# Performance work log

Measured on AMD Instinct MI355X. Metric: run time of the kernel, lower is better.

Reference implementation:

```python
import jax, jax.numpy as jnp
import numpy as np

N_NODES = 100000
N_EDGES = 1600000
D_IN = 128
D_HID = 256
D_OUT = 128


def _glorot(key, shape):
    fan_in, fan_out = shape[1], shape[0]
    lim = (6.0 / (fan_in + fan_out)) ** 0.5
    return jax.random.uniform(key, shape, jnp.float32, -lim, lim)


def setup_inputs() -> dict:
    key = jax.random.key(0)
    ks = jax.random.split(key, 8)
    x = jax.random.normal(ks[0], (N_NODES, D_IN), jnp.float32)
    edge_index = jax.random.randint(ks[1], (2, N_EDGES), 0, N_NODES, jnp.int32)
    return {
        "x": x,
        "edge_index": edge_index,
        # layer 1: in=D_IN -> D_HID
        "Wl1": _glorot(ks[2], (D_HID, D_IN)), "bl1": jnp.zeros((D_HID,), jnp.float32),
        "Wr1": _glorot(ks[3], (D_HID, D_IN)),
        # layer 2: D_HID -> D_HID
        "Wl2": _glorot(ks[4], (D_HID, D_HID)), "bl2": jnp.zeros((D_HID,), jnp.float32),
        "Wr2": _glorot(ks[5], (D_HID, D_HID)),
        # layer 3: D_HID -> D_OUT
        "Wl3": _glorot(ks[6], (D_OUT, D_HID)), "bl3": jnp.zeros((D_OUT,), jnp.float32),
        "Wr3": _glorot(ks[7], (D_OUT, D_HID)),
    }


def _sage_conv(x, src, dst, inv_deg, Wl, bl, Wr):
    # PyG SAGEConv (aggr='mean'): out = lin_l(mean_j x_j) + lin_r(x_i)
    agg = jax.ops.segment_sum(x[src], dst, num_segments=N_NODES)  # [N, F]
    mean = agg * inv_deg[:, None]
    return mean @ Wl.T + bl + x @ Wr.T


def reference(x, edge_index, Wl1, bl1, Wr1, Wl2, bl2, Wr2, Wl3, bl3, Wr3):
    src, dst = edge_index[0], edge_index[1]
    deg = jax.ops.segment_sum(jnp.ones((src.shape[0],), jnp.float32), dst,
                              num_segments=N_NODES)
    inv_deg = jnp.where(deg > 0, 1.0 / jnp.maximum(deg, 1.0), 0.0)
    h = jax.nn.relu(_sage_conv(x, src, dst, inv_deg, Wl1, bl1, Wr1))
    h = jax.nn.relu(_sage_conv(h, src, dst, inv_deg, Wl2, bl2, Wr2))
    return _sage_conv(h, src, dst, inv_deg, Wl3, bl3, Wr3)
```

## Files before the change

kernel.cpp:

```cpp
#include <hip/hip_runtime.h>

#define NN 100000
#define NE 1600000
#define DIN 128
#define DHID 256
#define DOUT 128
#define CAP 64

typedef unsigned int u32;
typedef unsigned short u16;

typedef __bf16 bf16x8 __attribute__((ext_vector_type(8)));
typedef float  f32x4  __attribute__((ext_vector_type(4)));

__device__ inline u16 f2bf(float f) {
    u32 u = __float_as_uint(f);
    u32 r = u + 0x7FFFu + ((u >> 16) & 1u);
    return (u16)(r >> 16);
}
__device__ inline u32 pack2(float a, float b) {
    return (u32)f2bf(a) | ((u32)f2bf(b) << 16);
}
__device__ inline float bflo(u32 u) { return __uint_as_float(u << 16); }
__device__ inline float bfhi(u32 u) { return __uint_as_float(u & 0xffff0000u); }

__global__ void csr_build(const int* __restrict__ src, const int* __restrict__ dst,
                          int* __restrict__ fill, int* __restrict__ csrC, int nE) {
    int g  = blockIdx.x & 7;
    int bg = blockIdx.x >> 3;
    int nbg = gridDim.x >> 3;
    int lo = g * (NN / 8), hi = lo + (NN / 8);
    for (int e = bg * 256 + threadIdx.x; e < nE; e += nbg * 256) {
        int d = __builtin_nontemporal_load(dst + e);
        if (d >= lo && d < hi) {
            int pos = atomicAdd(&fill[d], 1);
            if (pos < CAP) csrC[(size_t)d * CAP + pos] = __builtin_nontemporal_load(src + e);
        }
    }
}

__global__ void invdeg_from_fill(const int* __restrict__ fill, float* __restrict__ invdeg, int n) {
    int i = blockIdx.x * 256 + threadIdx.x;
    if (i < n) { int d = fill[i]; invdeg[i] = d > 0 ? 1.0f / (float)d : 0.0f; }
}

__global__ void f32_to_bf16(const float4* __restrict__ in, uint2* __restrict__ outp, int total4) {
    int i = blockIdx.x * 256 + threadIdx.x;
    if (i < total4) {
        float4 v = in[i];
        uint2 r; r.x = pack2(v.x, v.y); r.y = pack2(v.z, v.w);
        outp[i] = r;
    }
}

__global__ void weights_to_bf16(const float4* __restrict__ W0, const float4* __restrict__ W1,
                                const float4* __restrict__ W2, const float4* __restrict__ W3,
                                const float4* __restrict__ W4, const float4* __restrict__ W5,
                                uint2* __restrict__ outp) {
    int i = blockIdx.x * 256 + threadIdx.x;
    if (i >= 65536) return;
    const float4* p; int off;
    if (i < 8192)       { p = W0; off = i; }
    else if (i < 16384) { p = W1; off = i - 8192; }
    else if (i < 32768) { p = W2; off = i - 16384; }
    else if (i < 49152) { p = W3; off = i - 32768; }
    else if (i < 57344) { p = W4; off = i - 49152; }
    else                { p = W5; off = i - 57344; }
    float4 v = p[off];
    uint2 r; r.x = pack2(v.x, v.y); r.y = pack2(v.z, v.w);
    outp[i] = r;
}

#define ACC8(A, U) \
    A[0] += bflo(U.x); A[1] += bfhi(U.x); A[2] += bflo(U.y); A[3] += bfhi(U.y); \
    A[4] += bflo(U.z); A[5] += bfhi(U.z); A[6] += bflo(U.w); A[7] += bfhi(U.w);

__global__ __launch_bounds__(256)
void agg128_u4(const uint4* __restrict__ feat,
               const int* __restrict__ fill, const float* __restrict__ invdeg,
               const int* __restrict__ csrC, uint4* __restrict__ aggOut) {
    int w = (blockIdx.x * 256 + threadIdx.x) >> 6;
    int lane = threadIdx.x & 63;
    if (w >= NN) return;
    int dg = fill[w]; if (dg > CAP) dg = CAP;
    const int* cp = csrC + (size_t)w * CAP;
    int q = lane >> 4, sub = lane & 15;
    float a[8] = {0,0,0,0,0,0,0,0};
    float b[8] = {0,0,0,0,0,0,0,0};
    int j = 0;
    for (; j + 7 < dg; j += 8) {
        int s0 = cp[j + q], s1 = cp[j + 4 + q];
        uint4 u0 = feat[(size_t)s0 * 16 + sub];
        uint4 u1 = feat[(size_t)s1 * 16 + sub];
        ACC8(a, u0); ACC8(b, u1);
    }
    while (j < dg) {
        if (j + q < dg) {
            int s0 = cp[j + q];
            uint4 u0 = feat[(size_t)s0 * 16 + sub];
            ACC8(a, u0);
        }
        j += 4;
    }
    float iv = invdeg[w];
#pragma unroll
    for (int i = 0; i < 8; ++i) {
        float v = a[i] + b[i];
        v += __shfl_xor(v, 16, 64);
        v += __shfl_xor(v, 32, 64);
        a[i] = v * iv;
    }
    if (q == 0) {
        uint4 r;
        r.x = pack2(a[0], a[1]); r.y = pack2(a[2], a[3]);
        r.z = pack2(a[4], a[5]); r.w = pack2(a[6], a[7]);
        aggOut[(size_t)w * 16 + sub] = r;
    }
}

__global__ __launch_bounds__(256)
void agg256_u4(const uint4* __restrict__ feat,
               const int* __restrict__ fill, const float* __restrict__ invdeg,
               const int* __restrict__ csrC, uint4* __restrict__ aggOut) {
    int w = (blockIdx.x * 256 + threadIdx.x) >> 6;
    int lane = threadIdx.x & 63;
    if (w >= NN) return;
    int dg = fill[w]; if (dg > CAP) dg = CAP;
    const int* cp = csrC + (size_t)w * CAP;
    int h = lane >> 5, sub = lane & 31;
    float a[8] = {0,0,0,0,0,0,0,0};
    float b[8] = {0,0,0,0,0,0,0,0};
    float c[8] = {0,0,0,0,0,0,0,0};
    float d[8] = {0,0,0,0,0,0,0,0};
    int j = 0;
    for (; j + 7 < dg; j += 8) {
        int s0 = cp[j + h],     s1 = cp[j + 2 + h];
        int s2 = cp[j + 4 + h], s3 = cp[j + 6 + h];
        uint4 u0 = feat[(size_t)s0 * 32 + sub];
        uint4 u1 = feat[(size_t)s1 * 32 + sub];
        uint4 u2 = feat[(size_t)s2 * 32 + sub];
        uint4 u3 = feat[(size_t)s3 * 32 + sub];
        ACC8(a, u0); ACC8(b, u1); ACC8(c, u2); ACC8(d, u3);
    }
    while (j < dg) {
        if (j + h < dg) {
            int s0 = cp[j + h];
            uint4 u0 = feat[(size_t)s0 * 32 + sub];
            ACC8(a, u0);
        }
        j += 2;
    }
    float iv = invdeg[w];
#pragma unroll
    for (int i = 0; i < 8; ++i) {
        float v = (a[i] + b[i]) + (c[i] + d[i]);
        v += __shfl_xor(v, 32, 64);
        a[i] = v * iv;
    }
    if (h == 0) {
        uint4 r;
        r.x = pack2(a[0], a[1]); r.y = pack2(a[2], a[3]);
        r.z = pack2(a[4], a[5]); r.w = pack2(a[6], a[7]);
        aggOut[(size_t)w * 32 + sub] = r;
    }
}

template<int SH, int OFF>
__global__ __launch_bounds__(256)
void agg_bf16(const u32* __restrict__ feat,
              const int* __restrict__ fill, const float* __restrict__ invdeg,
              const int* __restrict__ csrC, u32* __restrict__ aggOut) {
    int w = (blockIdx.x * 256 + threadIdx.x) >> 6;
    int lane = threadIdx.x & 63;
    if (w >= NN) return;
    int dg = fill[w]; if (dg > CAP) dg = CAP;
    const int* cp = csrC + (size_t)w * CAP;
    float a0 = 0.f, b0 = 0.f, a1 = 0.f, b1 = 0.f;
    int j = 0;
    for (; j + 1 < dg; j += 2) {
        int s0 = cp[j], s1 = cp[j+1];
        u32 u0 = feat[((size_t)s0 << SH) + OFF + lane];
        u32 u1 = feat[((size_t)s1 << SH) + OFF + lane];
        a0 += bflo(u0); b0 += bfhi(u0);
        a1 += bflo(u1); b1 += bfhi(u1);
    }
    if (j < dg) {
        u32 u0 = feat[((size_t)cp[j] << SH) + OFF + lane];
        a0 += bflo(u0); b0 += bfhi(u0);
    }
    float iv = invdeg[w];
    aggOut[(size_t)w * 64 + lane] = pack2((a0 + a1) * iv, (b0 + b1) * iv);
}

#define TM 128
#define TN 128
#define TK 32
#define LDSTR 40

__device__ inline void mfma_pass_bf(const u16* __restrict__ A, int K, int lda,
                                    const u16* __restrict__ Wb, int ldw,
                                    int brow, int bcol, int n,
                                    int tid, int lane, int wr, int wc,
                                    u16* As, u16* Ws, f32x4 (&acc)[4][4])
{
    int rsel = lane & 15;
    int krun = (lane >> 4) << 3;
    int r0 = tid >> 2,         k80 = (tid & 3) << 3;
    int r1 = (tid + 256) >> 2, k81 = k80;
    uint4 av0, av1, wv0, wv1;
    const uint4 zero4 = make_uint4(0u, 0u, 0u, 0u);

    av0 = (brow + r0 < n) ? *(const uint4*)(A + (size_t)(brow + r0) * lda + k80) : zero4;
    av1 = (brow + r1 < n) ? *(const uint4*)(A + (size_t)(brow + r1) * lda + k81) : zero4;
    wv0 = *(const uint4*)(Wb + (size_t)(bcol + r0) * ldw + k80);
    wv1 = *(const uint4*)(Wb + (size_t)(bcol + r1) * ldw + k81);

    for (int kt = 0; kt < K; kt += TK) {
        __syncthreads();
        *(uint4*)&As[r0 * LDSTR + k80] = av0;
        *(uint4*)&As[r1 * LDSTR + k81] = av1;
        *(uint4*)&Ws[r0 * LDSTR + k80] = wv0;
        *(uint4*)&Ws[r1 * LDSTR + k81] = wv1;
        __syncthreads();
        int kn = kt + TK;
        if (kn < K) {
            av0 = (brow + r0 < n) ? *(const uint4*)(A + (size_t)(brow + r0) * lda + kn + k80) : zero4;
            av1 = (brow + r1 < n) ? *(const uint4*)(A + (size_t)(brow + r1) * lda + kn + k81) : zero4;
            wv0 = *(const uint4*)(Wb + (size_t)(bcol + r0) * ldw + kn + k80);
            wv1 = *(const uint4*)(Wb + (size_t)(bcol + r1) * ldw + kn + k81);
        }
        bf16x8 a[4], b[4];
#pragma unroll
        for (int mb = 0; mb < 4; ++mb)
            a[mb] = *(const bf16x8*)&As[(64 * wr + 16 * mb + rsel) * LDSTR + krun];
#pragma unroll
        for (int nb = 0; nb < 4; ++nb)
            b[nb] = *(const bf16x8*)&Ws[(64 * wc + 16 * nb + rsel) * LDSTR + krun];
#pragma unroll
        for (int mb = 0; mb < 4; ++mb)
#pragma unroll
            for (int nb = 0; nb < 4; ++nb)
                acc[mb][nb] = __builtin_amdgcn_mfma_f32_16x16x32_bf16(
                    a[mb], b[nb], acc[mb][nb], 0, 0, 0);
    }
}

template<int CF32, int RELU, int ACCUM>
__global__ __launch_bounds__(256)
void gemm_mfma(const u16* __restrict__ A1, int K1, int lda1,
               const u16* __restrict__ W1, int ldw1,
               const u16* __restrict__ A2, int K2, int lda2,
               const u16* __restrict__ W2, int ldw2,
               const float* __restrict__ bias, const u16* __restrict__ accBuf,
               void* __restrict__ C, int n, int cout)
{
    __shared__ u16 As[TM * LDSTR];
    __shared__ u16 Ws[TN * LDSTR];
    int tid = threadIdx.x;
    int lane = tid & 63, wid = tid >> 6;
    int wr = wid >> 1, wc = wid & 1;
    int brow = blockIdx.x * TM, bcol = blockIdx.y * TN;

    f32x4 acc[4][4];
#pragma unroll
    for (int i = 0; i < 4; ++i)
#pragma unroll
        for (int j = 0; j < 4; ++j) acc[i][j] = (f32x4){0.f, 0.f, 0.f, 0.f};

    mfma_pass_bf(A1, K1, lda1, W1, ldw1, brow, bcol, n, tid, lane, wr, wc, As, Ws, acc);
    if (K2 > 0)
        mfma_pass_bf(A2, K2, lda2, W2, ldw2, brow, bcol, n, tid, lane, wr, wc, As, Ws, acc);

    int rsel = lane & 15;
    int rgrp = (lane >> 4) << 2;
    float bv[4];
#pragma unroll
    for (int nb = 0; nb < 4; ++nb)
        bv[nb] = bias ? bias[bcol + 64 * wc + 16 * nb + rsel] : 0.f;

#pragma unroll
    for (int mb = 0; mb < 4; ++mb) {
        int rowb = brow + 64 * wr + 16 * mb + rgrp;
#pragma unroll
        for (int r = 0; r < 4; ++r) {
            int row = rowb + r;
            if (row >= n) continue;
            size_t rof = (size_t)row * cout;
#pragma unroll
            for (int nb = 0; nb < 4; ++nb) {
                int col = bcol + 64 * wc + 16 * nb + rsel;
                float v = acc[mb][nb][r] + bv[nb];
                if (ACCUM == 2) v += __uint_as_float(((u32)accBuf[rof + col]) << 16);
                if (CF32) {
                    float* p = (float*)C + rof + col;
                    if (ACCUM == 1) v += *p;
                    if (RELU) v = fmaxf(v, 0.f);
                    *p = v;
                } else {
                    u16* p = (u16*)C + rof + col;
                    if (ACCUM == 1) v += __uint_as_float(((u32)(*p)) << 16);
                    if (RELU) v = fmaxf(v, 0.f);
                    *p = f2bf(v);
                }
            }
        }
    }
}

extern "C" void kernel_launch(void* const* d_in, const int* in_sizes, int n_in,
                              void* d_out, int out_size, void* d_ws, size_t ws_size,
                              hipStream_t stream) {
    const float* x   = (const float*)d_in[0];
    const int*   ei  = (const int*)d_in[1];
    const float* Wl1 = (const float*)d_in[2];
    const float* bl1 = (const float*)d_in[3];
    const float* Wr1 = (const float*)d_in[4];
    const float* Wl2 = (const float*)d_in[5];
    const float* bl2 = (const float*)d_in[6];
    const float* Wr2 = (const float*)d_in[7];
    const float* Wl3 = (const float*)d_in[8];
    const float* bl3 = (const float*)d_in[9];
    const float* Wr3 = (const float*)d_in[10];
    float* out = (float*)d_out;

    const int* src = ei;
    const int* dst = ei + NE;

    char* ws = (char*)d_ws;
    int*   fill   = (int*)  (ws + 0);
    float* invdeg = (float*)(ws + 400000);
    int*   csrC   = (int*)  (ws + 800000);
    u16*   Wb     = (u16*)  (ws + 26400000);
    u16*   aggS   = (u16*)  (ws + 26924288);
    u16*   h2     = (u16*)  (ws + 52524288);
    u16*   h1     = (u16*)  (ws + 103724288);
    u16*   agg256 = (u16*)  (ws + 154924288);
    u16*   x_bf   = h2;
    u16*   t3     = h1;

    const bool big = ws_size >= 206124288ull;

    u16* wbL1 = Wb + 0;
    u16* wbR1 = Wb + 32768;
    u16* wbL2 = Wb + 65536;
    u16* wbR2 = Wb + 131072;
    u16* wbL3 = Wb + 196608;
    u16* wbR3 = Wb + 229376;

    dim3 b256(256);
    dim3 gN((NN + 255) / 256);
    dim3 gC((NN * 32 + 255) / 256);
    dim3 gW((NN * 64 + 255) / 256);
    dim3 gg2((NN + TM - 1) / TM, DHID / TN);
    dim3 gg1((NN + TM - 1) / TM, DOUT / TN);

    hipLaunchKernelGGL(weights_to_bf16, dim3(256), b256, 0, stream,
                       (const float4*)Wl1, (const float4*)Wr1, (const float4*)Wl2,
                       (const float4*)Wr2, (const float4*)Wl3, (const float4*)Wr3,
                       (uint2*)Wb);

    hipMemsetAsync(fill, 0, 400000, stream);
    hipLaunchKernelGGL(csr_build, dim3(2048), b256, 0, stream, src, dst, fill, csrC, NE);
    hipLaunchKernelGGL(invdeg_from_fill, gN, b256, 0, stream, fill, invdeg, NN);

    hipLaunchKernelGGL(f32_to_bf16, gC, b256, 0, stream,
                       (const float4*)x, (uint2*)x_bf, NN * 32);

    hipLaunchKernelGGL(agg128_u4, gW, b256, 0, stream,
                       (const uint4*)x_bf, fill, invdeg, csrC, (uint4*)aggS);
    hipLaunchKernelGGL((gemm_mfma<0, 1, 0>), gg2, b256, 0, stream,
                       aggS, DIN, DIN, wbL1, DIN,
                       x_bf, DIN, DIN, wbR1, DIN,
                       bl1, nullptr, h1, NN, DHID);

    if (big) {
        hipLaunchKernelGGL(agg256_u4, gW, b256, 0, stream,
                           (const uint4*)h1, fill, invdeg, csrC, (uint4*)agg256);
        hipLaunchKernelGGL((gemm_mfma<0, 1, 0>), gg2, b256, 0, stream,
                           agg256, DHID, DHID, wbL2, DHID,
                           h1, DHID, DHID, wbR2, DHID,
                           bl2, nullptr, h2, NN, DHID);
    } else {
        hipLaunchKernelGGL((agg_bf16<7, 0>), gW, b256, 0, stream,
                           (const u32*)h1, fill, invdeg, csrC, (u32*)aggS);
        hipLaunchKernelGGL((gemm_mfma<0, 0, 0>), gg2, b256, 0, stream,
                           aggS, 128, 128, wbL2, DHID,
                           h1, DHID, DHID, wbR2, DHID,
                           bl2, nullptr, h2, NN, DHID);
        hipLaunchKernelGGL((agg_bf16<7, 64>), gW, b256, 0, stream,
                           (const u32*)h1, fill, invdeg, csrC, (u32*)aggS);
        hipLaunchKernelGGL((gemm_mfma<0, 1, 1>), gg2, b256, 0, stream,
                           aggS, 128, 128, wbL2 + 128, DHID,
                           nullptr, 0, 0, nullptr, 0,
                           nullptr, nullptr, h2, NN, DHID);
    }

    hipLaunchKernelGGL((gemm_mfma<0, 0, 0>), gg1, b256, 0, stream,
                       h2, DHID, DHID, wbL3, DHID,
                       nullptr, 0, 0, nullptr, 0,
                       nullptr, nullptr, t3, NN, DOUT);
    hipLaunchKernelGGL(agg128_u4, gW, b256, 0, stream,
                       (const uint4*)t3, fill, invdeg, csrC, (uint4*)aggS);
    hipLaunchKernelGGL((gemm_mfma<1, 0, 2>), gg1, b256, 0, stream,
                       h2, DHID, DHID, wbR3, DHID,
                       nullptr, 0, 0, nullptr, 0,
                       bl3, aggS, out, NN, DOUT);
}
```

Before: 485.7 us.

## Slice feature columns across blocks in aggregation and widen GEMM N-tile to 256

The aggregation kernels are replaced by one templated kernel. Each block now handles a 64-byte column slice of four nodes, and 16 neighbors are gathered in parallel per wave, so gathered rows are split across blocks instead of one wave reading the whole row. The layer-1/2 GEMMs use 512-thread blocks covering all 256 output columns, so each A tile is loaded once rather than twice. The changes trade more blocks and shuffle reductions for more memory parallelism, and they add register and LDS pressure in the bigger GEMM tile.

New measurement: 943.0 us. 1.94x slower.

```diff
diff --git a/kernel.cpp b/kernel.cpp
--- a/kernel.cpp
+++ b/kernel.cpp
@@ -75,93 +75,42 @@
     A[0] += bflo(U.x); A[1] += bfhi(U.x); A[2] += bflo(U.y); A[3] += bfhi(U.y); \
     A[4] += bflo(U.z); A[5] += bfhi(U.z); A[6] += bflo(U.w); A[7] += bfhi(U.w);
 
+template<int NSL>
 __global__ __launch_bounds__(256)
-void agg128_u4(const uint4* __restrict__ feat,
-               const int* __restrict__ fill, const float* __restrict__ invdeg,
-               const int* __restrict__ csrC, uint4* __restrict__ aggOut) {
-    int w = (blockIdx.x * 256 + threadIdx.x) >> 6;
+void agg_sl(const uint4* __restrict__ feat,
+            const int* __restrict__ fill, const float* __restrict__ invdeg,
+            const int* __restrict__ csrC, uint4* __restrict__ aggOut) {
+    int s = blockIdx.x % NSL;
+    int chunk = blockIdx.x / NSL;
+    int w = chunk * 4 + (threadIdx.x >> 6);
     int lane = threadIdx.x & 63;
     if (w >= NN) return;
     int dg = fill[w]; if (dg > CAP) dg = CAP;
     const int* cp = csrC + (size_t)w * CAP;
-    int q = lane >> 4, sub = lane & 15;
+    int g = lane >> 2, sub = lane & 3;
     float a[8] = {0,0,0,0,0,0,0,0};
-    float b[8] = {0,0,0,0,0,0,0,0};
-    int j = 0;
-    for (; j + 7 < dg; j += 8) {
-        int s0 = cp[j + q], s1 = cp[j + 4 + q];
-        uint4 u0 = feat[(size_t)s0 * 16 + sub];
-        uint4 u1 = feat[(size_t)s1 * 16 + sub];
-        ACC8(a, u0); ACC8(b, u1);
-    }
-    while (j < dg) {
-        if (j + q < dg) {
-            int s0 = cp[j + q];
-            uint4 u0 = feat[(size_t)s0 * 16 + sub];
-            ACC8(a, u0);
-        }
-        j += 4;
+    for (int j = 0; j < dg; j += 16) {
+        if (j + g < dg) {
+            int sn = cp[j + g];
+            uint4 u = feat[(size_t)sn * (NSL * 4) + s * 4 + sub];
+            ACC8(a, u);
+        }
     }
     float iv = invdeg[w];
 #pragma unroll
     for (int i = 0; i < 8; ++i) {
-        float v = a[i] + b[i];
-        v += __shfl_xor(v, 16, 64);
-        v += __shfl_xor(v, 32, 64);
+        float v = a[i];
+        v += __shfl_xor(v, 4);
+        v += __shfl_xor(v, 8);
+        v += __shfl_xor(v, 16);
+        v += __shfl_xor(v, 32);
         a[i] = v * iv;
     }
-    if (q == 0) {
+    if (g == 0) {
         uint4 r;
         r.x = pack2(a[0], a[1]); r.y = pack2(a[2], a[3]);
         r.z = pack2(a[4], a[5]); r.w = pack2(a[6], a[7]);
-        aggOut[(size_t)w * 16 + sub] = r;
-    }
-}
-
-__global__ __launch_bounds__(256)
-void agg256_u4(const uint4* __restrict__ feat,
-               const int* __restrict__ fill, const float* __restrict__ invdeg,
-               const int* __restrict__ csrC, uint4* __restrict__ aggOut) {
-    int w = (blockIdx.x * 256 + threadIdx.x) >> 6;
-    int lane = threadIdx.x & 63;
-    if (w >= NN) return;
-    int dg = fill[w]; if (dg > CAP) dg = CAP;
-    const int* cp = csrC + (size_t)w * CAP;
-    int h = lane >> 5, sub = lane & 31;
-    float a[8] = {0,0,0,0,0,0,0,0};
-    float b[8] = {0,0,0,0,0,0,0,0};
-    float c[8] = {0,0,0,0,0,0,0,0};
-    float d[8] = {0,0,0,0,0,0,0,0};
-    int j = 0;
-    for (; j + 7 < dg; j += 8) {
-        int s0 = cp[j + h],     s1 = cp[j + 2 + h];
-        int s2 = cp[j + 4 + h], s3 = cp[j + 6 + h];
-        uint4 u0 = feat[(size_t)s0 * 32 + sub];
-        uint4 u1 = feat[(size_t)s1 * 32 + sub];
-        uint4 u2 = feat[(size_t)s2 * 32 + sub];
-        uint4 u3 = feat[(size_t)s3 * 32 + sub];
-        ACC8(a, u0); ACC8(b, u1); ACC8(c, u2); ACC8(d, u3);
-    }
-    while (j < dg) {
-        if (j + h < dg) {
-            int s0 = cp[j + h];
-            uint4 u0 = feat[(size_t)s0 * 32 + sub];
-            ACC8(a, u0);
-        }
-        j += 2;
-    }
-    float iv = invdeg[w];
-#pragma unroll
-    for (int i = 0; i < 8; ++i) {
-        float v = (a[i] + b[i]) + (c[i] + d[i]);
-        v += __shfl_xor(v, 32, 64);
-        a[i] = v * iv;
-    }
-    if (h == 0) {
-        uint4 r;
-        r.x = pack2(a[0], a[1]); r.y = pack2(a[2], a[3]);
-        r.z = pack2(a[4], a[5]); r.w = pack2(a[6], a[7]);
-        aggOut[(size_t)w * 32 + sub] = r;
+        aggOut[(size_t)w * (NSL * 4) + s * 4 + sub] = r;
     }
 }
 
@@ -193,41 +142,59 @@
 }
 
 #define TM 128
-#define TN 128
 #define TK 32
 #define LDSTR 40
 
+template<int NT, int TNN>
 __device__ inline void mfma_pass_bf(const u16* __restrict__ A, int K, int lda,
                                     const u16* __restrict__ Wb, int ldw,
                                     int brow, int bcol, int n,
                                     int tid, int lane, int wr, int wc,
                                     u16* As, u16* Ws, f32x4 (&acc)[4][4])
 {
+    constexpr int ACH = (TM * TK) / (8 * NT);
+    constexpr int WCH = (TNN * TK) / (8 * NT);
     int rsel = lane & 15;
     int krun = (lane >> 4) << 3;
-    int r0 = tid >> 2,         k80 = (tid & 3) << 3;
-    int r1 = (tid + 256) >> 2, k81 = k80;
-    uint4 av0, av1, wv0, wv1;
     const uint4 zero4 = make_uint4(0u, 0u, 0u, 0u);
-
-    av0 = (brow + r0 < n) ? *(const uint4*)(A + (size_t)(brow + r0) * lda + k80) : zero4;
-    av1 = (brow + r1 < n) ? *(const uint4*)(A + (size_t)(brow + r1) * lda + k81) : zero4;
-    wv0 = *(const uint4*)(Wb + (size_t)(bcol + r0) * ldw + k80);
-    wv1 = *(const uint4*)(Wb + (size_t)(bcol + r1) * ldw + k81);
+    uint4 av[ACH], wv[WCH];
+
+#pragma unroll
+    for (int i = 0; i < ACH; ++i) {
+        int c = tid + i * NT, r = c >> 2, k8 = (c & 3) << 3;
+        av[i] = (brow + r < n) ? *(const uint4*)(A + (size_t)(brow + r) * lda + k8) : zero4;
+    }
+#pragma unroll
+    for (int i = 0; i < WCH; ++i) {
+        int c = tid + i * NT, r = c >> 2, k8 = (c & 3) << 3;
+        wv[i] = *(const uint4*)(Wb + (size_t)(bcol + r) * ldw + k8);
+    }
 
     for (int kt = 0; kt < K; kt += TK) {
         __syncthreads();
-        *(uint4*)&As[r0 * LDSTR + k80] = av0;
-        *(uint4*)&As[r1 * LDSTR + k81] = av1;
-        *(uint4*)&Ws[r0 * LDSTR + k80] = wv0;
-        *(uint4*)&Ws[r1 * LDSTR + k81] = wv1;
+#pragma unroll
+        for (int i = 0; i < ACH; ++i) {
+            int c = tid + i * NT, r = c >> 2, k8 = (c & 3) << 3;
+            *(uint4*)&As[r * LDSTR + k8] = av[i];
+        }
+#pragma unroll
+        for (int i = 0; i < WCH; ++i) {
+            int c = tid + i * NT, r = c >> 2, k8 = (c & 3) << 3;
+            *(uint4*)&Ws[r * LDSTR + k8] = wv[i];
+        }
         __syncthreads();
         int kn = kt + TK;
         if (kn < K) {
-            av0 = (brow + r0 < n) ? *(const uint4*)(A + (size_t)(brow + r0) * lda + kn + k80) : zero4;
-            av1 = (brow + r1 < n) ? *(const uint4*)(A + (size_t)(brow + r1) * lda + kn + k81) : zero4;
-            wv0 = *(const uint4*)(Wb + (size_t)(bcol + r0) * ldw + kn + k80);
-            wv1 = *(const uint4*)(Wb + (size_t)(bcol + r1) * ldw + kn + k81);
+#pragma unroll
+            for (int i = 0; i < ACH; ++i) {
+                int c = tid + i * NT, r = c >> 2, k8 = (c & 3) << 3;
+                av[i] = (brow + r < n) ? *(const uint4*)(A + (size_t)(brow + r) * lda + kn + k8) : zero4;
+            }
+#pragma unroll
+            for (int i = 0; i < WCH; ++i) {
+                int c = tid + i * NT, r = c >> 2, k8 = (c & 3) << 3;
+                wv[i] = *(const uint4*)(Wb + (size_t)(bcol + r) * ldw + kn + k8);
+            }
         }
         bf16x8 a[4], b[4];
 #pragma unroll
@@ -245,8 +212,8 @@
     }
 }
 
-template<int CF32, int RELU, int ACCUM>
-__global__ __launch_bounds__(256)
+template<int NT, int TNN, int CF32, int RELU, int ACCUM>
+__global__ __launch_bounds__(NT)
 void gemm_mfma(const u16* __restrict__ A1, int K1, int lda1,
                const u16* __restrict__ W1, int ldw1,
                const u16* __restrict__ A2, int K2, int lda2,
@@ -254,12 +221,13 @@
                const float* __restrict__ bias, const u16* __restrict__ accBuf,
                void* __restrict__ C, int n, int cout)
 {
+    constexpr int NWC = TNN / 64;
     __shared__ u16 As[TM * LDSTR];
-    __shared__ u16 Ws[TN * LDSTR];
+    __shared__ u16 Ws[TNN * LDSTR];
     int tid = threadIdx.x;
     int lane = tid & 63, wid = tid >> 6;
-    int wr = wid >> 1, wc = wid & 1;
-    int brow = blockIdx.x * TM, bcol = blockIdx.y * TN;
+    int wr = wid / NWC, wc = wid % NWC;
+    int brow = blockIdx.x * TM, bcol = blockIdx.y * TNN;
 
     f32x4 acc[4][4];
 #pragma unroll
@@ -267,9 +235,9 @@
 #pragma unroll
         for (int j = 0; j < 4; ++j) acc[i][j] = (f32x4){0.f, 0.f, 0.f, 0.f};
 
-    mfma_pass_bf(A1, K1, lda1, W1, ldw1, brow, bcol, n, tid, lane, wr, wc, As, Ws, acc);
+    mfma_pass_bf<NT, TNN>(A1, K1, lda1, W1, ldw1, brow, bcol, n, tid, lane, wr, wc, As, Ws, acc);
     if (K2 > 0)
-        mfma_pass_bf(A2, K2, lda2, W2, ldw2, brow, bcol, n, tid, lane, wr, wc, As, Ws, acc);
+        mfma_pass_bf<NT, TNN>(A2, K2, lda2, W2, ldw2, brow, bcol, n, tid, lane, wr, wc, As, Ws, acc);
 
     int rsel = lane & 15;
     int rgrp = (lane >> 4) << 2;
@@ -351,8 +319,12 @@
     dim3 gN((NN + 255) / 256);
     dim3 gC((NN * 32 + 255) / 256);
     dim3 gW((NN * 64 + 255) / 256);
-    dim3 gg2((NN + TM - 1) / TM, DHID / TN);
-    dim3 gg1((NN + TM - 1) / TM, DOUT / TN);
+    const int CHUNKS = (NN + 3) / 4;
+    dim3 gS4(CHUNKS * 4);
+    dim3 gS8(CHUNKS * 8);
+    dim3 ggL1((NN + TM - 1) / TM, 1);
+    dim3 gg1((NN + TM - 1) / TM, 1);
+    dim3 gg2f((NN + TM - 1) / TM, 2);
 
     hipLaunchKernelGGL(weights_to_bf16, dim3(256), b256, 0, stream,
                        (const float4*)Wl1, (const float4*)Wr1, (const float4*)Wl2,
@@ -366,42 +338,42 @@
     hipLaunchKernelGGL(f32_to_bf16, gC, b256, 0, stream,
                        (const float4*)x, (uint2*)x_bf, NN * 32);
 
-    hipLaunchKernelGGL(agg128_u4, gW, b256, 0, stream,
+    hipLaunchKernelGGL((agg_sl<4>), gS4, b256, 0, stream,
                        (const uint4*)x_bf, fill, invdeg, csrC, (uint4*)aggS);
-    hipLaunchKernelGGL((gemm_mfma<0, 1, 0>), gg2, b256, 0, stream,
+    hipLaunchKernelGGL((gemm_mfma<512, 256, 0, 1, 0>), ggL1, dim3(512), 0, stream,
                        aggS, DIN, DIN, wbL1, DIN,
                        x_bf, DIN, DIN, wbR1, DIN,
                        bl1, nullptr, h1, NN, DHID);
 
     if (big) {
-        hipLaunchKernelGGL(agg256_u4, gW, b256, 0, stream,
+        hipLaunchKernelGGL((agg_sl<8>), gS8, b256, 0, stream,
                            (const uint4*)h1, fill, invdeg, csrC, (uint4*)agg256);
-        hipLaunchKernelGGL((gemm_mfma<0, 1, 0>), gg2, b256, 0, stream,
+        hipLaunchKernelGGL((gemm_mfma<512, 256, 0, 1, 0>), ggL1, dim3(512), 0, stream,
                            agg256, DHID, DHID, wbL2, DHID,
                            h1, DHID, DHID, wbR2, DHID,
                            bl2, nullptr, h2, NN, DHID);
     } else {
         hipLaunchKernelGGL((agg_bf16<7, 0>), gW, b256, 0, stream,
                            (const u32*)h1, fill, invdeg, csrC, (u32*)aggS);
-        hipLaunchKernelGGL((gemm_mfma<0, 0, 0>), gg2, b256, 0, stream,
+        hipLaunchKernelGGL((gemm_mfma<256, 128, 0, 0, 0>), gg2f, b256, 0, stream,
                            aggS, 128, 128, wbL2, DHID,
                            h1, DHID, DHID, wbR2, DHID,
                            bl2, nullptr, h2, NN, DHID);
         hipLaunchKernelGGL((agg_bf16<7, 64>), gW, b256, 0, stream,
                            (const u32*)h1, fill, invdeg, csrC, (u32*)aggS);
-        hipLaunchKernelGGL((gemm_mfma<0, 1, 1>), gg2, b256, 0, stream,
+        hipLaunchKernelGGL((gemm_mfma<256, 128, 0, 1, 1>), gg2f, b256, 0, stream,
                            aggS, 128, 128, wbL2 + 128, DHID,
                            nullptr, 0, 0, nullptr, 0,
                            nullptr, nullptr, h2, NN, DHID);
     }
 
-    hipLaunchKernelGGL((gemm_mfma<0, 0, 0>), gg1, b256, 0, stream,
+    hipLaunchKernelGGL((gemm_mfma<256, 128, 0, 0, 0>), gg1, b256, 0, stream,
                        h2, DHID, DHID, wbL3, DHID,
                        nullptr, 0, 0, nullptr, 0,
                        nullptr, nullptr, t3, NN, DOUT);
-    hipLaunchKernelGGL(agg128_u4, gW, b256, 0, stream,
+    hipLaunchKernelGGL((agg_sl<4>), gS4, b256, 0, stream,
                        (const uint4*)t3, fill, invdeg, csrC, (uint4*)aggS);
-    hipLaunchKernelGGL((gemm_mfma<1, 0, 2>), gg1, b256, 0, stream,
+    hipLaunchKernelGGL((gemm_mfma<256, 128, 1, 0, 2>), gg1, b256, 0, stream,
                        h2, DHID, DHID, wbR3, DHID,
                        nullptr, 0, 0, nullptr, 0,
                        bl3, aggS, out, NN, DOUT);
```
